# Optimization experiments

Measured on AMD Instinct MI355X. Metric: run time of the kernel, lower is better.

## Reference

```python
import jax, jax.numpy as jnp
import numpy as np
import math

DIMS, K_SIZE, V_SIZE = 1024, 128, 128

def setup_inputs() -> dict:
    key = jax.random.key(0)
    ks = jax.random.split(key, 7)
    B, S = 4, 2048
    scale = 1.0 / math.sqrt(DIMS)
    return {
        "inputs": jax.random.normal(ks[0], (B, S, DIMS), dtype=jnp.float32),
        "Wq": jax.random.normal(ks[1], (DIMS, K_SIZE), dtype=jnp.float32) * scale,
        "bq": jnp.zeros((K_SIZE,), dtype=jnp.float32),
        "Wk": jax.random.normal(ks[2], (DIMS, K_SIZE), dtype=jnp.float32) * scale,
        "bk": jnp.zeros((K_SIZE,), dtype=jnp.float32),
        "Wv": jax.random.normal(ks[3], (DIMS, V_SIZE), dtype=jnp.float32) * scale,
        "bv": jnp.zeros((V_SIZE,), dtype=jnp.float32),
    }

def reference(inputs, Wq, bq, Wk, bk, Wv, bv):
    # inputs: [B, S, D]
    q = inputs @ Wq + bq            # [B, S, k]
    k = inputs @ Wk + bk            # [B, S, k]
    v = inputs @ Wv + bv            # [B, S, v]
    logits = jnp.einsum('bqk,bsk->bqs', q, k)  # [B, S, S]
    S = inputs.shape[1]
    causal = jnp.tril(jnp.ones((S, S), dtype=bool))  # allow j <= i (triu k=1 masked)
    logits = jnp.where(causal, logits, -jnp.inf)
    probs = jax.nn.softmax(logits / jnp.sqrt(jnp.float32(Wk.shape[1])), axis=-1)
    read = jnp.einsum('bqs,bsv->bqv', probs, v)  # [B, S, v]
    return jnp.concatenate([inputs, read], axis=-1)  # [B, S, D+v]
```

## Files before the change

kernel.cpp:

```cpp
#include <hip/hip_runtime.h>
#include <hip/hip_bf16.h>

typedef __attribute__((ext_vector_type(8))) short bf16x8;
typedef __attribute__((ext_vector_type(4))) float f32x4;
typedef __attribute__((ext_vector_type(8))) unsigned short u16x8;
typedef __attribute__((ext_vector_type(4))) float float4_t;

static constexpr int Bn = 4, Sn = 2048, Dn = 1024, Kn = 128;
static constexpr int ODn = Dn + Kn;
static constexpr int CH = 4;
static constexpr int CPB = 144;
static constexpr float L2E = 1.4426950408889634f;

__device__ __forceinline__ unsigned short f2bf(float f) {
    union { float f; unsigned int u; } v; v.f = f;
    unsigned int u = v.u;
    return (unsigned short)((u + 0x7fffu + ((u >> 16) & 1u)) >> 16);
}
__device__ __forceinline__ float bf2f(unsigned short h) {
    union { float f; unsigned int u; } v; v.u = ((unsigned int)h) << 16;
    return v.f;
}

#define GLOAD16(g, l) __builtin_amdgcn_global_load_lds( \
    (const __attribute__((address_space(1))) void*)(g), \
    (__attribute__((address_space(3))) void*)(l), 16, 0, 0)

__global__ __launch_bounds__(256) void wt_prep(const float* __restrict__ Wq,
                                               const float* __restrict__ Wk,
                                               const float* __restrict__ Wv,
                                               unsigned short* __restrict__ Wt) {
    __shared__ unsigned short tile[32][34];
    int k0 = blockIdx.x * 32, c0 = blockIdx.y * 32, w = blockIdx.z;
    const float* W = (w == 0) ? Wq : (w == 1) ? Wk : Wv;
    int tc = threadIdx.x & 31;
    int tr = (threadIdx.x >> 5) * 4;
#pragma unroll
    for (int i = 0; i < 4; ++i)
        tile[tr + i][tc] = f2bf(W[(size_t)(k0 + tr + i) * Kn + c0 + tc]);
    __syncthreads();
    unsigned short* dst = Wt + (size_t)w * Kn * Dn;
#pragma unroll
    for (int i = 0; i < 4; ++i)
        dst[(size_t)(c0 + tr + i) * Dn + k0 + tc] = tile[tc][tr + i];
}

__global__ __launch_bounds__(256, 2) void proj_kernel(
    const float* __restrict__ X, const unsigned short* __restrict__ Wt,
    const float* __restrict__ bq, const float* __restrict__ bk, const float* __restrict__ bv,
    float* __restrict__ out,
    unsigned short* __restrict__ qws, unsigned short* __restrict__ kws,
    unsigned short* __restrict__ vtws) {
    __shared__ __align__(16) unsigned short Alds[2][64 * 64];
    __shared__ __align__(16) unsigned short Wlds[3][96 * 64];
    constexpr int NT = 16;
    const int orig = blockIdx.x;
    const int wg = (orig & 7) * 64 + (orig >> 3);
    const int m0 = (wg >> 2) * 64;
    const int ns = wg & 3;
    const int c0 = ns * 96;
    const int t = threadIdx.x, lane = t & 63, wn = t >> 6;
    const int lr = lane & 15, lg = lane >> 4;
    const int wr = wn >> 1, wc = wn & 1;
    const int ar0 = t >> 3, ach = t & 7;

    const unsigned short* wsrcp[3]; int wdst[3];
#pragma unroll
    for (int p = 0; p < 3; ++p) {
        int s = t + p * 256, col = s >> 3, kseg = s & 7;
        wsrcp[p] = Wt + (size_t)(c0 + col) * Dn + ((kseg ^ (col & 7)) * 8);
        wdst[p] = col * 128 + kseg * 16;
    }
    const float* xbase = X + (size_t)(m0 + ar0) * Dn + ach * 8;
    float* obase = out + (size_t)(m0 + ar0) * ODn + ach * 8;
    f32x4 acc[2][3] = {};
    float4_t va0[4], va1[4];

    auto loadA = [&](float4_t* va, int j) {
        const int k0 = j * 64;
        va[0] = *(const float4_t*)(xbase + k0);
        va[1] = *(const float4_t*)(xbase + k0 + 4);
        va[2] = *(const float4_t*)(xbase + (size_t)32 * Dn + k0);
        va[3] = *(const float4_t*)(xbase + (size_t)32 * Dn + k0 + 4);
    };
    auto stageW = [&](int wbuf, int j) {
#pragma unroll
        for (int p = 0; p < 3; ++p)
            GLOAD16(wsrcp[p] + j * 64, (char*)&Wlds[wbuf][0] + wdst[p]);
    };
    auto writeA = [&](const float4_t* va, int abuf, int j) {
        const int k0 = j * 64;
        if ((j >> 2) == ns) {
            *(float4_t*)(obase + k0) = va[0];
            *(float4_t*)(obase + k0 + 4) = va[1];
            *(float4_t*)(obase + (size_t)32 * ODn + k0) = va[2];
            *(float4_t*)(obase + (size_t)32 * ODn + k0 + 4) = va[3];
        }
        u16x8 h0, h1;
#pragma unroll
        for (int jj = 0; jj < 4; ++jj) {
            h0[jj] = f2bf(va[0][jj]); h0[jj + 4] = f2bf(va[1][jj]);
            h1[jj] = f2bf(va[2][jj]); h1[jj + 4] = f2bf(va[3][jj]);
        }
        const int r1 = ar0 + 32;
        *(u16x8*)((char*)&Alds[abuf][0] + ar0 * 128 + ((ach * 16) ^ ((ar0 & 7) << 4))) = h0;
        *(u16x8*)((char*)&Alds[abuf][0] + r1 * 128 + ((ach * 16) ^ ((r1 & 7) << 4))) = h1;
    };
    auto compute = [&](int abuf, int wbuf) {
        __builtin_amdgcn_s_setprio(1);
#pragma unroll
        for (int kk = 0; kk < 2; ++kk) {
            bf16x8 afr[2], bfr[3];
#pragma unroll
            for (int mi = 0; mi < 2; ++mi) {
                int row = wr * 32 + mi * 16 + lr;
                afr[mi] = *(const bf16x8*)((const char*)&Alds[abuf][0] +
                           row * 128 + ((kk * 64 + lg * 16) ^ ((row & 7) << 4)));
            }
#pragma unroll
            for (int ni = 0; ni < 3; ++ni) {
                int col = wc * 48 + ni * 16 + lr;
                bfr[ni] = *(const bf16x8*)((const char*)&Wlds[wbuf][0] +
                           col * 128 + ((kk * 64 + lg * 16) ^ ((col & 7) << 4)));
            }
#pragma unroll
            for (int mi = 0; mi < 2; ++mi)
#pragma unroll
                for (int ni = 0; ni < 3; ++ni)
                    acc[mi][ni] = __builtin_amdgcn_mfma_f32_16x16x32_bf16(afr[mi], bfr[ni], acc[mi][ni], 0, 0, 0);
        }
        __builtin_amdgcn_s_setprio(0);
    };

    loadA(va0, 0);  stageW(0, 0);
    loadA(va1, 1);  stageW(1, 1);
    writeA(va0, 0, 0);
    asm volatile("s_waitcnt vmcnt(7) lgkmcnt(0)" ::: "memory");
    __builtin_amdgcn_sched_barrier(0);
    __builtin_amdgcn_s_barrier();
    __builtin_amdgcn_sched_barrier(0);

    for (int ii = 0; ii < 14; ii += 2) {
        loadA(va0, ii + 2);  stageW((ii + 2) % 3, ii + 2);
        compute(0, ii % 3);
        writeA(va1, 1, ii + 1);
        asm volatile("s_waitcnt vmcnt(7) lgkmcnt(0)" ::: "memory");
        __builtin_amdgcn_sched_barrier(0);
        __builtin_amdgcn_s_barrier();
        __builtin_amdgcn_sched_barrier(0);
        loadA(va1, ii + 3);  stageW((ii + 3) % 3, ii + 3);
        compute(1, (ii + 1) % 3);
        writeA(va0, 0, ii + 2);
        asm volatile("s_waitcnt vmcnt(7) lgkmcnt(0)" ::: "memory");
        __builtin_amdgcn_sched_barrier(0);
        __builtin_amdgcn_s_barrier();
        __builtin_amdgcn_sched_barrier(0);
    }
    compute(0, 14 % 3);
    writeA(va1, 1, 15);
    asm volatile("s_waitcnt vmcnt(0) lgkmcnt(0)" ::: "memory");
    __builtin_amdgcn_sched_barrier(0);
    __builtin_amdgcn_s_barrier();
    __builtin_amdgcn_sched_barrier(0);
    compute(1, 15 % 3);

#pragma unroll
    for (int ni = 0; ni < 3; ++ni) {
        int gcol = c0 + wc * 48 + ni * 16 + lr;
        int buf = gcol >> 7, ci = gcol & 127;
        float bias = (buf == 0 ? bq : buf == 1 ? bk : bv)[ci];
#pragma unroll
        for (int mi = 0; mi < 2; ++mi) {
#pragma unroll
            for (int r = 0; r < 4; ++r) {
                int grow = m0 + wr * 32 + mi * 16 + lg * 4 + r;
                unsigned short hv = f2bf(acc[mi][ni][r] + bias);
                if (buf == 0) qws[(size_t)grow * Kn + ci] = hv;
                else if (buf == 1) kws[(size_t)grow * Kn + ci] = hv;
                else {
                    int bb = grow >> 11, ss = grow & 2047;
                    vtws[((size_t)bb * Kn + ci) * Sn + ss] = hv;
                }
            }
        }
    }
}

__global__ __launch_bounds__(256, 2) void attn_kernel(
    const unsigned short* __restrict__ qws, const unsigned short* __restrict__ kws,
    const unsigned short* __restrict__ vtws,
    unsigned short* __restrict__ part_o, float* __restrict__ part_ml) {
    __shared__ __align__(16) unsigned short Klds[2][64 * 128];
    __shared__ __align__(16) unsigned short Vlds[2][128 * 64];
    __shared__ __align__(16) unsigned short Plds[4][16 * 64];
    constexpr float SCALE = 0.08838834764831845f;
    const int t = threadIdx.x, lane = t & 63, wid = t >> 6;
    const int lr = lane & 15, lg = lane >> 4;
    const int pidx = blockIdx.x;
    const int b = pidx / CPB;
    const int idx = pidx - b * CPB;
    int qt = 0, rem = idx;
    while (true) { int n = (qt + CH) >> 2; if (rem < n) break; rem -= n; ++qt; }
    const int c = rem;
    const int it0 = c * CH;
    const int it1 = (it0 + CH < qt + 1) ? (it0 + CH) : (qt + 1);
    const int qrow0 = qt * 64 + wid * 16;

    const unsigned short* kb  = kws  + (size_t)b * Sn * Kn;
    const unsigned short* vtb = vtws + (size_t)b * Kn * Sn;
    const unsigned short* ksrc[4];
    const unsigned short* vsrc[4];
#pragma unroll
    for (int p = 0; p < 4; ++p) {
        int row = wid * 16 + p * 4 + (lane >> 4);
        int seg = lane & 15;
        ksrc[p] = kb + (size_t)row * Kn + ((seg ^ (row & 7)) * 8);
        int cc = wid * 32 + p * 8 + (lane >> 3);
        int sg = lane & 7;
        vsrc[p] = vtb + (size_t)cc * Sn + ((sg ^ (cc & 7)) * 8);
    }
    auto stage = [&](int buf, int it) {
#pragma unroll
        for (int p = 0; p < 4; ++p) {
            GLOAD16(ksrc[p] + (size_t)it * (64 * Kn), (char*)&Klds[buf][0] + wid * 4096 + p * 1024);
            GLOAD16(vsrc[p] + (size_t)it * 64,        (char*)&Vlds[buf][0] + wid * 4096 + p * 1024);
        }
    };

    const unsigned short* qbase = qws + ((size_t)b * Sn + qrow0) * Kn;
    bf16x8 qf[4];
#pragma unroll
    for (int kk = 0; kk < 4; ++kk)
        qf[kk] = *(const bf16x8*)(qbase + (size_t)lr * Kn + kk * 32 + lg * 8);
    f32x4 o[8] = {};
    float mrow[4] = {-1e30f, -1e30f, -1e30f, -1e30f};
    float lrow[4] = {0.f, 0.f, 0.f, 0.f};

    stage(0, it0);
    __syncthreads();

    for (int it = it0; it < it1; ++it) {
        const int cur = (it - it0) & 1;
        if (it + 1 < it1) stage(cur ^ 1, it + 1);
        const int kv0 = it * 64;
        f32x4 s[4] = {};
        __builtin_amdgcn_s_setprio(1);
#pragma unroll
        for (int n = 0; n < 4; ++n) {
            int kvr = n * 16 + lr;
#pragma unroll
            for (int kk = 0; kk < 4; ++kk) {
                int off = (kvr * 256 + kk * 64 + lg * 16) ^ ((kvr & 7) << 4);
                bf16x8 kf = *(const bf16x8*)((const char*)&Klds[cur][0] + off);
                s[n] = __builtin_amdgcn_mfma_f32_16x16x32_bf16(qf[kk], kf, s[n], 0, 0, 0);
            }
        }
        __builtin_amdgcn_s_setprio(0);
        if (it == qt) {
#pragma unroll
            for (int n = 0; n < 4; ++n) {
                int kvg = kv0 + n * 16 + lr;
#pragma unroll
                for (int r = 0; r < 4; ++r) {
                    float sv = s[n][r] * SCALE;
                    int qg = qrow0 + lg * 4 + r;
                    s[n][r] = (kvg > qg) ? -1e30f : sv;
                }
            }
        } else {
#pragma unroll
            for (int n = 0; n < 4; ++n)
#pragma unroll
                for (int r = 0; r < 4; ++r)
                    s[n][r] *= SCALE;
        }
        float tmax[4], rsum[4];
#pragma unroll
        for (int r = 0; r < 4; ++r)
            tmax[r] = fmaxf(fmaxf(s[0][r], s[1][r]), fmaxf(s[2][r], s[3][r]));
#pragma unroll
        for (int d = 1; d < 16; d <<= 1)
#pragma unroll
            for (int r = 0; r < 4; ++r)
                tmax[r] = fmaxf(tmax[r], __shfl_xor(tmax[r], d));
        float need = fmaxf(fmaxf(tmax[0] - mrow[0], tmax[1] - mrow[1]),
                           fmaxf(tmax[2] - mrow[2], tmax[3] - mrow[3]));
        if (!__all(need <= 8.0f)) {
#pragma unroll
            for (int r = 0; r < 4; ++r) {
                float mnew = fmaxf(mrow[r], tmax[r]);
                float alpha = exp2f((mrow[r] - mnew) * L2E);
                mrow[r] = mnew;
                lrow[r] *= alpha;
#pragma unroll
                for (int v = 0; v < 8; ++v)
                    o[v][r] *= alpha;
            }
        }
        unsigned short pb[4][4];
#pragma unroll
        for (int r = 0; r < 4; ++r) rsum[r] = 0.f;
#pragma unroll
        for (int n = 0; n < 4; ++n)
#pragma unroll
            for (int r = 0; r < 4; ++r) {
                float p = exp2f((s[n][r] - mrow[r]) * L2E);
                rsum[r] += p;
                pb[n][r] = f2bf(p);
            }
#pragma unroll
        for (int d = 1; d < 16; d <<= 1)
#pragma unroll
            for (int r = 0; r < 4; ++r)
                rsum[r] += __shfl_xor(rsum[r], d);
#pragma unroll
        for (int r = 0; r < 4; ++r)
            lrow[r] += rsum[r];
        char* pbase = (char*)&Plds[wid][0];
#pragma unroll
        for (int n = 0; n < 4; ++n)
#pragma unroll
            for (int r = 0; r < 4; ++r) {
                int q = lg * 4 + r, kv = n * 16 + lr;
                int off = (q * 128 + kv * 2) ^ ((q & 7) << 4);
                *(unsigned short*)(pbase + off) = pb[n][r];
            }
        bf16x8 pa[2];
#pragma unroll
        for (int kk = 0; kk < 2; ++kk) {
            int aoff = (lr * 128 + kk * 64 + lg * 16) ^ ((lr & 7) << 4);
            pa[kk] = *(const bf16x8*)((const char*)pbase + aoff);
        }
        __builtin_amdgcn_s_setprio(1);
#pragma unroll
        for (int v = 0; v < 8; ++v) {
            int vcol = v * 16 + lr;
#pragma unroll
            for (int kk = 0; kk < 2; ++kk) {
                int boff = (vcol * 128 + kk * 64 + lg * 16) ^ ((vcol & 7) << 4);
                bf16x8 vb = *(const bf16x8*)((const char*)&Vlds[cur][0] + boff);
                o[v] = __builtin_amdgcn_mfma_f32_16x16x32_bf16(pa[kk], vb, o[v], 0, 0, 0);
            }
        }
        __builtin_amdgcn_s_setprio(0);
        __syncthreads();
    }
    const size_t pbo = (size_t)pidx * (64 * 128);
#pragma unroll
    for (int v = 0; v < 8; ++v)
#pragma unroll
        for (int r = 0; r < 4; ++r) {
            int row = wid * 16 + lg * 4 + r;
            part_o[pbo + (size_t)row * 128 + v * 16 + lr] = f2bf(o[v][r]);
        }
    if (lr == 0) {
#pragma unroll
        for (int r = 0; r < 4; ++r) {
            int row = wid * 16 + lg * 4 + r;
            part_ml[(size_t)pidx * 128 + row * 2]     = mrow[r];
            part_ml[(size_t)pidx * 128 + row * 2 + 1] = lrow[r];
        }
    }
}

__global__ __launch_bounds__(256) void reduce_kernel(
    const unsigned short* __restrict__ part_o, const float* __restrict__ part_ml,
    float* __restrict__ out) {
    const int bid = blockIdx.x;
    const int rh = bid & 1, bq = bid >> 1;
    const int qt = bq & 31, b = bq >> 5;
    const int nch = (qt + CH) >> 2;
    int idx0 = 0;
    for (int q = 0; q < qt; ++q) idx0 += (q + CH) >> 2;
    const int pidx0 = b * CPB + idx0;
    const int t = threadIdx.x;
    const int row = rh * 32 + (t >> 3);
    const int col0 = (t & 7) * 16;

    float mc[8], lc[8];
#pragma unroll
    for (int cc = 0; cc < 8; ++cc) { mc[cc] = -1e30f; lc[cc] = 0.f; }
#pragma unroll
    for (int cc = 0; cc < 8; ++cc)
        if (cc < nch) {
            mc[cc] = part_ml[(size_t)(pidx0 + cc) * 128 + row * 2];
            lc[cc] = part_ml[(size_t)(pidx0 + cc) * 128 + row * 2 + 1];
        }
    float m = -1e30f;
#pragma unroll
    for (int cc = 0; cc < 8; ++cc) m = fmaxf(m, mc[cc]);
    float l = 0.f;
    float accv[16] = {};
#pragma unroll
    for (int cc = 0; cc < 8; ++cc)
        if (cc < nch) {
            float w = exp2f((mc[cc] - m) * L2E);
            l += w * lc[cc];
            const unsigned short* po = part_o + (size_t)(pidx0 + cc) * (64 * 128) + (size_t)row * 128 + col0;
            bf16x8 v0 = *(const bf16x8*)(po);
            bf16x8 v1 = *(const bf16x8*)(po + 8);
#pragma unroll
            for (int j = 0; j < 8; ++j) {
                accv[j]     += w * bf2f((unsigned short)v0[j]);
                accv[8 + j] += w * bf2f((unsigned short)v1[j]);
            }
        }
    const float inv = 1.f / l;
    float* op = out + ((size_t)b * Sn + qt * 64 + row) * ODn + Dn + col0;
#pragma unroll
    for (int j = 0; j < 4; ++j) {
        float4_t v = { accv[j*4] * inv, accv[j*4+1] * inv, accv[j*4+2] * inv, accv[j*4+3] * inv };
        *(float4_t*)(op + j * 4) = v;
    }
}

extern "C" void kernel_launch(void* const* d_in, const int* in_sizes, int n_in,
                              void* d_out, int out_size, void* d_ws, size_t ws_size,
                              hipStream_t stream) {
    const float* X  = (const float*)d_in[0];
    const float* Wq = (const float*)d_in[1];
    const float* bq = (const float*)d_in[2];
    const float* Wk = (const float*)d_in[3];
    const float* bk = (const float*)d_in[4];
    const float* Wv = (const float*)d_in[5];
    const float* bv = (const float*)d_in[6];
    float* out = (float*)d_out;

    unsigned short* Wt   = (unsigned short*)d_ws;
    unsigned short* qws  = Wt  + (size_t)3 * Kn * Dn;
    unsigned short* kws  = qws + (size_t)Bn * Sn * Kn;
    unsigned short* vtws = kws + (size_t)Bn * Sn * Kn;
    unsigned short* part_o = vtws + (size_t)Bn * Sn * Kn;
    float* part_ml = (float*)(part_o + (size_t)Bn * CPB * 64 * 128);

    wt_prep<<<dim3(32, 4, 3), 256, 0, stream>>>(Wq, Wk, Wv, Wt);
    proj_kernel<<<512, 256, 0, stream>>>(X, Wt, bq, bk, bv, out, qws, kws, vtws);
    attn_kernel<<<Bn * CPB, 256, 0, stream>>>(qws, kws, vtws, part_o, part_ml);
    reduce_kernel<<<256, 256, 0, stream>>>(part_o, part_ml, out);
}
```

Before: 66.85 us.

## Retile QKV projection to 64-wide column tiles with 3-deep A prefetch

The projection kernel now splits the 384 output columns into six 64-wide tiles instead of four 96-wide tiles, launching 768 blocks with a higher occupancy target of 3 blocks per SM. Each wave computes a 16x64 strip, and X loads are triple-buffered in registers with adjusted waitcnt thresholds. The passthrough copy of X into the output is moved to a separate upfront copy loop done by the first four column tiles. The aim is more parallelism and better latency hiding, at the cost of each X tile being re-read by six blocks instead of four.

Result: slower. 68.47 us (+2.4%).

```diff
diff --git a/kernel.cpp b/kernel.cpp
--- a/kernel.cpp
+++ b/kernel.cpp
@@ -45,62 +45,65 @@
         dst[(size_t)(c0 + tr + i) * Dn + k0 + tc] = tile[tc][tr + i];
 }
 
-__global__ __launch_bounds__(256, 2) void proj_kernel(
+__global__ __launch_bounds__(256, 3) void proj_kernel(
     const float* __restrict__ X, const unsigned short* __restrict__ Wt,
     const float* __restrict__ bq, const float* __restrict__ bk, const float* __restrict__ bv,
     float* __restrict__ out,
     unsigned short* __restrict__ qws, unsigned short* __restrict__ kws,
     unsigned short* __restrict__ vtws) {
     __shared__ __align__(16) unsigned short Alds[2][64 * 64];
-    __shared__ __align__(16) unsigned short Wlds[3][96 * 64];
-    constexpr int NT = 16;
+    __shared__ __align__(16) unsigned short Wlds[3][64 * 64];
     const int orig = blockIdx.x;
-    const int wg = (orig & 7) * 64 + (orig >> 3);
-    const int m0 = (wg >> 2) * 64;
-    const int ns = wg & 3;
-    const int c0 = ns * 96;
+    const int wg = (orig & 7) * 96 + (orig >> 3);
+    const int m0 = (wg / 6) * 64;
+    const int ns = wg % 6;
+    const int c0 = ns * 64;
     const int t = threadIdx.x, lane = t & 63, wn = t >> 6;
     const int lr = lane & 15, lg = lane >> 4;
-    const int wr = wn >> 1, wc = wn & 1;
     const int ar0 = t >> 3, ach = t & 7;
 
-    const unsigned short* wsrcp[3]; int wdst[3];
-#pragma unroll
-    for (int p = 0; p < 3; ++p) {
-        int s = t + p * 256, col = s >> 3, kseg = s & 7;
+    if (ns < 4) {
+        const float* src = X + (size_t)m0 * Dn + ns * 256 + (t & 63) * 4;
+        float* dst = out + (size_t)m0 * ODn + ns * 256 + (t & 63) * 4;
+        const int r0 = t >> 6;
+#pragma unroll
+        for (int itc = 0; itc < 16; ++itc) {
+            const int r = itc * 4 + r0;
+            float4_t v = *(const float4_t*)(src + (size_t)r * Dn);
+            *(float4_t*)(dst + (size_t)r * ODn) = v;
+        }
+    }
+
+    const unsigned short* wsrcp[2]; int wdst[2];
+#pragma unroll
+    for (int p = 0; p < 2; ++p) {
+        int s = t + p * 256;
+        int col = s >> 3, kseg = s & 7;
         wsrcp[p] = Wt + (size_t)(c0 + col) * Dn + ((kseg ^ (col & 7)) * 8);
         wdst[p] = col * 128 + kseg * 16;
     }
     const float* xbase = X + (size_t)(m0 + ar0) * Dn + ach * 8;
-    float* obase = out + (size_t)(m0 + ar0) * ODn + ach * 8;
-    f32x4 acc[2][3] = {};
-    float4_t va0[4], va1[4];
-
-    auto loadA = [&](float4_t* va, int j) {
+    f32x4 acc[4] = {};
+    float4_t va[3][4];
+
+    auto loadA = [&](int slot, int j) {
         const int k0 = j * 64;
-        va[0] = *(const float4_t*)(xbase + k0);
-        va[1] = *(const float4_t*)(xbase + k0 + 4);
-        va[2] = *(const float4_t*)(xbase + (size_t)32 * Dn + k0);
-        va[3] = *(const float4_t*)(xbase + (size_t)32 * Dn + k0 + 4);
+        va[slot][0] = *(const float4_t*)(xbase + k0);
+        va[slot][1] = *(const float4_t*)(xbase + k0 + 4);
+        va[slot][2] = *(const float4_t*)(xbase + (size_t)32 * Dn + k0);
+        va[slot][3] = *(const float4_t*)(xbase + (size_t)32 * Dn + k0 + 4);
     };
     auto stageW = [&](int wbuf, int j) {
 #pragma unroll
-        for (int p = 0; p < 3; ++p)
+        for (int p = 0; p < 2; ++p)
             GLOAD16(wsrcp[p] + j * 64, (char*)&Wlds[wbuf][0] + wdst[p]);
     };
-    auto writeA = [&](const float4_t* va, int abuf, int j) {
-        const int k0 = j * 64;
-        if ((j >> 2) == ns) {
-            *(float4_t*)(obase + k0) = va[0];
-            *(float4_t*)(obase + k0 + 4) = va[1];
-            *(float4_t*)(obase + (size_t)32 * ODn + k0) = va[2];
-            *(float4_t*)(obase + (size_t)32 * ODn + k0 + 4) = va[3];
-        }
+    auto writeA = [&](int slot, int abuf) {
         u16x8 h0, h1;
 #pragma unroll
         for (int jj = 0; jj < 4; ++jj) {
-            h0[jj] = f2bf(va[0][jj]); h0[jj + 4] = f2bf(va[1][jj]);
-            h1[jj] = f2bf(va[2][jj]); h1[jj + 4] = f2bf(va[3][jj]);
+            h0[jj] = f2bf(va[slot][0][jj]); h0[jj + 4] = f2bf(va[slot][1][jj]);
+            h1[jj] = f2bf(va[slot][2][jj]); h1[jj + 4] = f2bf(va[slot][3][jj]);
         }
         const int r1 = ar0 + 32;
         *(u16x8*)((char*)&Alds[abuf][0] + ar0 * 128 + ((ach * 16) ^ ((ar0 & 7) << 4))) = h0;
@@ -110,77 +113,61 @@
         __builtin_amdgcn_s_setprio(1);
 #pragma unroll
         for (int kk = 0; kk < 2; ++kk) {
-            bf16x8 afr[2], bfr[3];
-#pragma unroll
-            for (int mi = 0; mi < 2; ++mi) {
-                int row = wr * 32 + mi * 16 + lr;
-                afr[mi] = *(const bf16x8*)((const char*)&Alds[abuf][0] +
-                           row * 128 + ((kk * 64 + lg * 16) ^ ((row & 7) << 4)));
-            }
-#pragma unroll
-            for (int ni = 0; ni < 3; ++ni) {
-                int col = wc * 48 + ni * 16 + lr;
-                bfr[ni] = *(const bf16x8*)((const char*)&Wlds[wbuf][0] +
-                           col * 128 + ((kk * 64 + lg * 16) ^ ((col & 7) << 4)));
-            }
-#pragma unroll
-            for (int mi = 0; mi < 2; ++mi)
-#pragma unroll
-                for (int ni = 0; ni < 3; ++ni)
-                    acc[mi][ni] = __builtin_amdgcn_mfma_f32_16x16x32_bf16(afr[mi], bfr[ni], acc[mi][ni], 0, 0, 0);
+            const int row = wn * 16 + lr;
+            bf16x8 afr = *(const bf16x8*)((const char*)&Alds[abuf][0] +
+                          row * 128 + ((kk * 64 + lg * 16) ^ ((row & 7) << 4)));
+#pragma unroll
+            for (int ni = 0; ni < 4; ++ni) {
+                int col = ni * 16 + lr;
+                bf16x8 bfr = *(const bf16x8*)((const char*)&Wlds[wbuf][0] +
+                              col * 128 + ((kk * 64 + lg * 16) ^ ((col & 7) << 4)));
+                acc[ni] = __builtin_amdgcn_mfma_f32_16x16x32_bf16(afr, bfr, acc[ni], 0, 0, 0);
+            }
         }
         __builtin_amdgcn_s_setprio(0);
     };
 
-    loadA(va0, 0);  stageW(0, 0);
-    loadA(va1, 1);  stageW(1, 1);
-    writeA(va0, 0, 0);
-    asm volatile("s_waitcnt vmcnt(7) lgkmcnt(0)" ::: "memory");
+    stageW(0, 0);
+    loadA(0, 0);
+    stageW(1, 1);
+    loadA(1, 1);
+    loadA(2, 2);
+    writeA(0, 0);
+    asm volatile("s_waitcnt vmcnt(10) lgkmcnt(0)" ::: "memory");
     __builtin_amdgcn_sched_barrier(0);
     __builtin_amdgcn_s_barrier();
     __builtin_amdgcn_sched_barrier(0);
 
-    for (int ii = 0; ii < 14; ii += 2) {
-        loadA(va0, ii + 2);  stageW((ii + 2) % 3, ii + 2);
-        compute(0, ii % 3);
-        writeA(va1, 1, ii + 1);
-        asm volatile("s_waitcnt vmcnt(7) lgkmcnt(0)" ::: "memory");
-        __builtin_amdgcn_sched_barrier(0);
-        __builtin_amdgcn_s_barrier();
-        __builtin_amdgcn_sched_barrier(0);
-        loadA(va1, ii + 3);  stageW((ii + 3) % 3, ii + 3);
-        compute(1, (ii + 1) % 3);
-        writeA(va0, 0, ii + 2);
-        asm volatile("s_waitcnt vmcnt(7) lgkmcnt(0)" ::: "memory");
-        __builtin_amdgcn_sched_barrier(0);
-        __builtin_amdgcn_s_barrier();
-        __builtin_amdgcn_sched_barrier(0);
-    }
-    compute(0, 14 % 3);
-    writeA(va1, 1, 15);
-    asm volatile("s_waitcnt vmcnt(0) lgkmcnt(0)" ::: "memory");
-    __builtin_amdgcn_sched_barrier(0);
-    __builtin_amdgcn_s_barrier();
-    __builtin_amdgcn_sched_barrier(0);
-    compute(1, 15 % 3);
-
-#pragma unroll
-    for (int ni = 0; ni < 3; ++ni) {
-        int gcol = c0 + wc * 48 + ni * 16 + lr;
+#pragma unroll
+    for (int i = 0; i < 16; ++i) {
+        if (i + 2 <= 15) stageW((i + 2) % 3, i + 2);
+        if (i + 3 <= 15) loadA((i + 3) % 3, i + 3);
+        compute(i & 1, i % 3);
+        if (i + 1 <= 15) writeA((i + 1) % 3, (i + 1) & 1);
+        if (i < 15) {
+            if (i <= 12)      asm volatile("s_waitcnt vmcnt(10) lgkmcnt(0)" ::: "memory");
+            else if (i == 13) asm volatile("s_waitcnt vmcnt(6) lgkmcnt(0)" ::: "memory");
+            else              asm volatile("s_waitcnt vmcnt(0) lgkmcnt(0)" ::: "memory");
+            __builtin_amdgcn_sched_barrier(0);
+            __builtin_amdgcn_s_barrier();
+            __builtin_amdgcn_sched_barrier(0);
+        }
+    }
+
+#pragma unroll
+    for (int ni = 0; ni < 4; ++ni) {
+        int gcol = c0 + ni * 16 + lr;
         int buf = gcol >> 7, ci = gcol & 127;
         float bias = (buf == 0 ? bq : buf == 1 ? bk : bv)[ci];
 #pragma unroll
-        for (int mi = 0; mi < 2; ++mi) {
-#pragma unroll
-            for (int r = 0; r < 4; ++r) {
-                int grow = m0 + wr * 32 + mi * 16 + lg * 4 + r;
-                unsigned short hv = f2bf(acc[mi][ni][r] + bias);
-                if (buf == 0) qws[(size_t)grow * Kn + ci] = hv;
-                else if (buf == 1) kws[(size_t)grow * Kn + ci] = hv;
-                else {
-                    int bb = grow >> 11, ss = grow & 2047;
-                    vtws[((size_t)bb * Kn + ci) * Sn + ss] = hv;
-                }
+        for (int r = 0; r < 4; ++r) {
+            int grow = m0 + wn * 16 + lg * 4 + r;
+            unsigned short hv = f2bf(acc[ni][r] + bias);
+            if (buf == 0) qws[(size_t)grow * Kn + ci] = hv;
+            else if (buf == 1) kws[(size_t)grow * Kn + ci] = hv;
+            else {
+                int bb = grow >> 11, ss = grow & 2047;
+                vtws[((size_t)bb * Kn + ci) * Sn + ss] = hv;
             }
         }
     }
@@ -434,7 +421,7 @@
     float* part_ml = (float*)(part_o + (size_t)Bn * CPB * 64 * 128);
 
     wt_prep<<<dim3(32, 4, 3), 256, 0, stream>>>(Wq, Wk, Wv, Wt);
-    proj_kernel<<<512, 256, 0, stream>>>(X, Wt, bq, bk, bv, out, qws, kws, vtws);
+    proj_kernel<<<768, 256, 0, stream>>>(X, Wt, bq, bk, bv, out, qws, kws, vtws);
     attn_kernel<<<Bn * CPB, 256, 0, stream>>>(qws, kws, vtws, part_o, part_ml);
     reduce_kernel<<<256, 256, 0, stream>>>(part_o, part_ml, out);
 }
```

## Stage attention K/V through registers instead of direct global-to-LDS loads

Applied to the files above, without the earlier changes.

Replaces the global_load_lds prefetch of the next K/V tile with ordinary global loads into registers issued at the top of the iteration, then writes them to the swizzled LDS buffer after the PV MFMAs. The XOR swizzle moves from the global source address to the LDS destination address. Launch bounds rise to 3 waves per SIMD to allow more occupancy. The register staging adds 8 bf16x8 live registers per thread, which may conflict with the tighter register budget.

Result: no change. 67.49 us (+1.0%).

```diff
diff --git a/kernel.cpp b/kernel.cpp
--- a/kernel.cpp
+++ b/kernel.cpp
@@ -53,7 +53,6 @@
     unsigned short* __restrict__ vtws) {
     __shared__ __align__(16) unsigned short Alds[2][64 * 64];
     __shared__ __align__(16) unsigned short Wlds[3][96 * 64];
-    constexpr int NT = 16;
     const int orig = blockIdx.x;
     const int wg = (orig & 7) * 64 + (orig >> 3);
     const int m0 = (wg >> 2) * 64;
@@ -186,7 +185,7 @@
     }
 }
 
-__global__ __launch_bounds__(256, 2) void attn_kernel(
+__global__ __launch_bounds__(256, 3) void attn_kernel(
     const unsigned short* __restrict__ qws, const unsigned short* __restrict__ kws,
     const unsigned short* __restrict__ vtws,
     unsigned short* __restrict__ part_o, float* __restrict__ part_ml) {
@@ -208,22 +207,32 @@
 
     const unsigned short* kb  = kws  + (size_t)b * Sn * Kn;
     const unsigned short* vtb = vtws + (size_t)b * Kn * Sn;
-    const unsigned short* ksrc[4];
-    const unsigned short* vsrc[4];
+    const unsigned short* gK[4]; const unsigned short* gV[4];
+    int dK[4], dV[4];
 #pragma unroll
     for (int p = 0; p < 4; ++p) {
         int row = wid * 16 + p * 4 + (lane >> 4);
         int seg = lane & 15;
-        ksrc[p] = kb + (size_t)row * Kn + ((seg ^ (row & 7)) * 8);
+        gK[p] = kb + (size_t)row * Kn + seg * 8;
+        dK[p] = row * 256 + ((seg ^ (row & 7)) << 4);
         int cc = wid * 32 + p * 8 + (lane >> 3);
         int sg = lane & 7;
-        vsrc[p] = vtb + (size_t)cc * Sn + ((sg ^ (cc & 7)) * 8);
-    }
-    auto stage = [&](int buf, int it) {
+        gV[p] = vtb + (size_t)cc * Sn + sg * 8;
+        dV[p] = cc * 128 + ((sg ^ (cc & 7)) << 4);
+    }
+    bf16x8 rK[4], rV[4];
+    auto loadRegs = [&](int it) {
 #pragma unroll
         for (int p = 0; p < 4; ++p) {
-            GLOAD16(ksrc[p] + (size_t)it * (64 * Kn), (char*)&Klds[buf][0] + wid * 4096 + p * 1024);
-            GLOAD16(vsrc[p] + (size_t)it * 64,        (char*)&Vlds[buf][0] + wid * 4096 + p * 1024);
+            rK[p] = *(const bf16x8*)(gK[p] + (size_t)it * (64 * Kn));
+            rV[p] = *(const bf16x8*)(gV[p] + (size_t)it * 64);
+        }
+    };
+    auto writeLds = [&](int buf) {
+#pragma unroll
+        for (int p = 0; p < 4; ++p) {
+            *(bf16x8*)((char*)&Klds[buf][0] + dK[p]) = rK[p];
+            *(bf16x8*)((char*)&Vlds[buf][0] + dV[p]) = rV[p];
         }
     };
 
@@ -236,12 +245,13 @@
     float mrow[4] = {-1e30f, -1e30f, -1e30f, -1e30f};
     float lrow[4] = {0.f, 0.f, 0.f, 0.f};
 
-    stage(0, it0);
+    loadRegs(it0);
+    writeLds(0);
     __syncthreads();
 
     for (int it = it0; it < it1; ++it) {
         const int cur = (it - it0) & 1;
-        if (it + 1 < it1) stage(cur ^ 1, it + 1);
+        if (it + 1 < it1) loadRegs(it + 1);
         const int kv0 = it * 64;
         f32x4 s[4] = {};
         __builtin_amdgcn_s_setprio(1);
@@ -343,6 +353,7 @@
             }
         }
         __builtin_amdgcn_s_setprio(0);
+        if (it + 1 < it1) writeLds(cur ^ 1);
         __syncthreads();
     }
     const size_t pbo = (size_t)pidx * (64 * 128);
```
